# Optimization experiments

Hardware: AMD Instinct MI355X
Metric: run time of the kernel (lower is better)

Reference implementation:

```python
import jax, jax.numpy as jnp
import numpy as np

N_NODES = 10000
N_EDGES = 160000
D_IN = 128
D_EMB = 512
D_HID = 256
GAT_SLOPE = 0.2   # PyG GATv2Conv default negative_slope
MLP_SLOPE = 0.1   # relu_alpha


def _glorot(key, shape):
    fan_in, fan_out = shape[0], shape[-1]
    lim = np.sqrt(6.0 / (fan_in + fan_out))
    return jax.random.uniform(key, shape, jnp.float32, -lim, lim)


def setup_inputs() -> dict:
    key = jax.random.key(0)
    ks = jax.random.split(key, 20)
    inp = {
        'x': jax.random.normal(ks[0], (N_NODES, D_IN), jnp.float32),
        'edge_index': jax.random.randint(ks[1], (2, N_EDGES), 0, N_NODES, jnp.int64),
    }
    # GATv2 layers: (Wl, Wr, att, bias) each
    dims = [(D_IN, D_EMB), (D_EMB, D_EMB), (D_EMB, D_EMB)]
    for i, (di, do) in enumerate(dims, start=1):
        inp[f'Wl{i}'] = _glorot(ks[2 + 4 * i], (di, do))
        inp[f'Wr{i}'] = _glorot(ks[3 + 4 * i], (di, do))
        inp[f'att{i}'] = _glorot(ks[4 + 4 * i], (1, do))[0]
        inp[f'b{i}'] = jnp.zeros((do,), jnp.float32)
    # MLP
    inp['A1'] = _glorot(ks[2], (D_EMB, D_HID)); inp['c1'] = jnp.zeros((D_HID,), jnp.float32)
    inp['A2'] = _glorot(ks[3], (D_HID, D_HID)); inp['c2'] = jnp.zeros((D_HID,), jnp.float32)
    inp['A3'] = _glorot(ks[4], (D_HID, 1));     inp['c3'] = jnp.zeros((1,), jnp.float32)
    return inp


def gatv2_conv(x, src, dst, Wl, Wr, att, bias):
    # PyG GATv2Conv, heads=1: xl = source transform, xr = target transform
    xl = x @ Wl                                   # [N, D]
    xr = x @ Wr                                   # [N, D]
    # per-edge attention logit: att . leaky_relu(xl[src] + xr[dst])
    e = jax.nn.leaky_relu(xl[src] + xr[dst], GAT_SLOPE) @ att   # [E]
    # segment softmax over incoming edges of each dst node
    emax = jax.ops.segment_max(e, dst, num_segments=N_NODES)    # [N]
    w = jnp.exp(e - emax[dst])
    denom = jax.ops.segment_sum(w, dst, num_segments=N_NODES)   # [N]
    alpha = w / (denom[dst] + 1e-16)                             # [E]
    out = jax.ops.segment_sum(alpha[:, None] * xl[src], dst, num_segments=N_NODES)
    return out + bias


def reference(x, edge_index, Wl1, Wr1, att1, b1, Wl2, Wr2, att2, b2,
              Wl3, Wr3, att3, b3, A1, c1, A2, c2, A3, c3):
    src, dst = edge_index[0], edge_index[1]
    h = jnp.tanh(gatv2_conv(x, src, dst, Wl1, Wr1, att1, b1))
    h = jnp.tanh(gatv2_conv(h, src, dst, Wl2, Wr2, att2, b2))
    h = jnp.tanh(gatv2_conv(h, src, dst, Wl3, Wr3, att3, b3))
    h = jax.nn.leaky_relu(h @ A1 + c1, MLP_SLOPE)
    h = jax.nn.leaky_relu(h @ A2 + c2, MLP_SLOPE)
    logits = h @ A3 + c3                          # [N, 1]
    return jax.nn.softmax(logits, axis=0)         # softmax over nodes
```

## Files before the change

kernel.cpp:

```cpp
#include <hip/hip_runtime.h>
#include <hip/hip_bf16.h>

#define N_NODES 10000
#define N_EDGES 160000
#define D_IN    128
#define D_EMB   512
#define D_HID   256

typedef unsigned short u16;
typedef __attribute__((ext_vector_type(8))) short short8;
typedef __attribute__((ext_vector_type(4))) float floatx4;

__device__ __forceinline__ float bf2f(u16 u) {
    union { unsigned int i; float f; } v; v.i = ((unsigned int)u) << 16; return v.f;
}
__device__ __forceinline__ u16 f2bf(float f) {
    union { float f; unsigned int i; } v; v.f = f;
    unsigned int x = v.i;
    return (u16)((x + 0x7fffu + ((x >> 16) & 1u)) >> 16);
}
__device__ __forceinline__ float inval(const void* p, int fp32, int idx) {
    return fp32 ? ((const float*)p)[idx] : bf2f(((const u16*)p)[idx]);
}

__device__ __forceinline__ void gld_lds16(const u16* g, u16* l) {
    __builtin_amdgcn_global_load_lds((const __attribute__((address_space(1))) void*)g,
                                     (__attribute__((address_space(3))) void*)l,
                                     16, 0, 0);
}

__device__ __forceinline__ int edge_src(const int* __restrict__ ei, int flg, int e) {
    int v = flg ? ei[2 * e] : ei[e];
    return min(max(v, 0), N_NODES - 1);
}
__device__ __forceinline__ int edge_dst(const int* __restrict__ ei, int flg, int e) {
    int v = flg ? ei[2 * N_EDGES + 2 * e] : ei[N_EDGES + e];
    return min(max(v, 0), N_NODES - 1);
}

__global__ void sentinel_kernel(float* out, int n) {
    int i = blockIdx.x * 256 + threadIdx.x;
    if (i < n) out[i] = 1.0f;
}

__global__ __launch_bounds__(256)
void detect_zero_kernel(const int* __restrict__ ei, const u16* __restrict__ xu,
                        int* flag, int* counts, float* logits) {
    int gid = blockIdx.x * 256 + threadIdx.x;
    for (int i = gid; i < N_NODES; i += gridDim.x * 256) { counts[i] = 0; logits[i] = 0.f; }
    if (blockIdx.x != 0) return;
    __shared__ int s_or[256];
    __shared__ int s_cnt[256];
    int t = threadIdx.x;
    int v = 0;
    for (int k = t; k < 4096; k += 256) v |= ei[1 + 2 * k];
    int c = 0;
    for (int k = t; k < 4096; k += 256) {
        u16 u = xu[k];
        int ex = (u >> 7) & 0xFF;
        bool plaus = (u == 0) || (ex >= 64 && ex <= 191);
        if (!plaus) c++;
    }
    s_or[t] = v; s_cnt[t] = c;
    __syncthreads();
    for (int off = 128; off > 0; off >>= 1) {
        if (t < off) { s_or[t] |= s_or[t + off]; s_cnt[t] += s_cnt[t + off]; }
        __syncthreads();
    }
    if (t == 0) {
        flag[0] = (s_or[0] == 0) ? 1 : 0;
        flag[1] = (s_cnt[0] > 256) ? 1 : 0;
    }
}

struct ConvJobs {
    const void* src[10];
    u16* dh[10];
    u16* dl[10];
    int rows[10], cols[10], trans[10];
    int cum[11];
    int njobs;
};

__global__ __launch_bounds__(256)
void convert_fused_kernel(ConvJobs jobs, const int* __restrict__ flag) {
    int idx = blockIdx.x * 256 + threadIdx.x;
    if (idx >= jobs.cum[jobs.njobs]) return;
    int fp32 = flag[1];
    int jb = 0;
    while (idx >= jobs.cum[jb + 1]) jb++;
    int local = idx - jobs.cum[jb];
    float v = inval(jobs.src[jb], fp32, local);
    u16 hi = f2bf(v);
    int o;
    if (jobs.trans[jb]) {
        int r = local / jobs.cols[jb], c = local % jobs.cols[jb];
        o = c * jobs.rows[jb] + r;
    } else o = local;
    jobs.dh[jb][o] = hi;
    if (jobs.dl[jb]) jobs.dl[jb][o] = f2bf(v - bf2f(hi));
}

__global__ void count_edges_kernel(const int* __restrict__ ei, const int* __restrict__ flag,
                                   int* counts) {
    int e = blockIdx.x * 256 + threadIdx.x;
    if (e < N_EDGES) atomicAdd(&counts[edge_dst(ei, flag[0], e)], 1);
}

__global__ __launch_bounds__(256)
void scan_counts_kernel(int* counts, int* rowptr) {
    __shared__ int part[256];
    int tid = threadIdx.x;
    const int CH = 40;
    int base = tid * CH;
    int loc[CH];
    int s = 0;
    #pragma unroll
    for (int i = 0; i < CH; i++) {
        int idx = base + i;
        int c = (idx < N_NODES) ? counts[idx] : 0;
        loc[i] = s; s += c;
    }
    part[tid] = s;
    __syncthreads();
    for (int off = 1; off < 256; off <<= 1) {
        int v = part[tid];
        int add = (tid >= off) ? part[tid - off] : 0;
        __syncthreads();
        part[tid] = v + add;
        __syncthreads();
    }
    int pre = (tid > 0) ? part[tid - 1] : 0;
    #pragma unroll
    for (int i = 0; i < CH; i++) {
        int idx = base + i;
        if (idx < N_NODES) { int v = pre + loc[i]; rowptr[idx] = v; counts[idx] = v; }
    }
    if (tid == 255) rowptr[N_NODES] = part[255];
}

__global__ void fill_esrcp_kernel(const int* __restrict__ ei, const int* __restrict__ flag,
                                  int* counts, int* esrcp) {
    int e = blockIdx.x * 256 + threadIdx.x;
    if (e < N_EDGES) {
        int flg = flag[0];
        int pos = atomicAdd(&counts[edge_dst(ei, flg, e)], 1);
        if (pos >= 0 && pos < N_EDGES) esrcp[pos] = edge_src(ei, flg, e);
    }
}

__global__ __launch_bounds__(256)
void gemm_dual_kernel(const u16* __restrict__ Ah, const u16* __restrict__ Al,
                      const u16* __restrict__ B0h, const u16* __restrict__ B1h,
                      u16* __restrict__ C0, float* __restrict__ C1,
                      int M, int N, int K)
{
    __shared__ u16 sAh[128 * 32];
    __shared__ u16 sAl[128 * 32];
    __shared__ u16 sBh[128 * 32];
    int nb = N >> 7;
    int half = (int)blockIdx.x >= nb;
    int bx = half ? (blockIdx.x - nb) : blockIdx.x;
    const u16* BTh = half ? B1h : B0h;

    int tid = threadIdx.x;
    int lane = tid & 63, wv = tid >> 6;
    int l15 = lane & 15, l4 = lane >> 4;
    int wr = (wv >> 1) * 64, wc = (wv & 1) * 64;
    int m0 = blockIdx.y * 128, n0 = bx * 128;

    int i0 = tid, i1 = tid + 256;
    int r0 = i0 >> 2, b0 = i0 & 3, sb0 = b0 ^ ((r0 >> 1) & 3);
    int r1 = i1 >> 2, b1 = i1 & 3, sb1 = b1 ^ ((r1 >> 1) & 3);
    int gr0 = min(m0 + r0, M - 1), gr1 = min(m0 + r1, M - 1);
    const u16* a0p = Ah + (size_t)gr0 * K + sb0 * 8;
    const u16* a1p = Ah + (size_t)gr1 * K + sb1 * 8;
    const u16* l0p = Al + (size_t)gr0 * K + sb0 * 8;
    const u16* l1p = Al + (size_t)gr1 * K + sb1 * 8;
    const u16* bb0p = BTh + (size_t)(n0 + r0) * K + sb0 * 8;
    const u16* bb1p = BTh + (size_t)(n0 + r1) * K + sb1 * 8;
    u16* lA0 = &sAh[(size_t)(wv * 64) * 8];
    u16* lA1 = &sAh[(size_t)(256 + wv * 64) * 8];
    u16* lL0 = &sAl[(size_t)(wv * 64) * 8];
    u16* lL1 = &sAl[(size_t)(256 + wv * 64) * 8];
    u16* lB0 = &sBh[(size_t)(wv * 64) * 8];
    u16* lB1 = &sBh[(size_t)(256 + wv * 64) * 8];

    floatx4 acc[4][4];
    #pragma unroll
    for (int i = 0; i < 4; i++)
        #pragma unroll
        for (int j = 0; j < 4; j++) acc[i][j] = (floatx4){0.f, 0.f, 0.f, 0.f};

    int aoff[4], boff[4];
    #pragma unroll
    for (int i = 0; i < 4; i++) {
        int arow = wr + i * 16 + l15;
        aoff[i] = arow * 32 + ((l4 ^ ((arow >> 1) & 3)) << 3);
        int bcol = wc + i * 16 + l15;
        boff[i] = bcol * 32 + ((l4 ^ ((bcol >> 1) & 3)) << 3);
    }

    for (int kk = 0; kk < K; kk += 32) {
        __syncthreads();
        gld_lds16(a0p + kk, lA0);
        gld_lds16(a1p + kk, lA1);
        gld_lds16(l0p + kk, lL0);
        gld_lds16(l1p + kk, lL1);
        gld_lds16(bb0p + kk, lB0);
        gld_lds16(bb1p + kk, lB1);
        __syncthreads();

        short8 ah[4], al[4];
        #pragma unroll
        for (int i = 0; i < 4; i++) {
            ah[i] = *(const short8*)(&sAh[aoff[i]]);
            al[i] = *(const short8*)(&sAl[aoff[i]]);
        }
        #pragma unroll
        for (int j = 0; j < 4; j++) {
            short8 bh = *(const short8*)(&sBh[boff[j]]);
            #pragma unroll
            for (int i = 0; i < 4; i++) {
                acc[i][j] = __builtin_amdgcn_mfma_f32_16x16x32_bf16(ah[i], bh, acc[i][j], 0, 0, 0);
                acc[i][j] = __builtin_amdgcn_mfma_f32_16x16x32_bf16(al[i], bh, acc[i][j], 0, 0, 0);
            }
        }
    }

    #pragma unroll
    for (int j = 0; j < 4; j++) {
        int col = n0 + wc + j * 16 + l15;
        #pragma unroll
        for (int i = 0; i < 4; i++) {
            #pragma unroll
            for (int r = 0; r < 4; r++) {
                int row = m0 + wr + i * 16 + l4 * 4 + r;
                if (row < M) {
                    if (half) C1[(size_t)row * N + col] = acc[i][j][r];
                    else      C0[(size_t)row * N + col] = f2bf(acc[i][j][r]);
                }
            }
        }
    }
}

template<int FUSE>
__global__ __launch_bounds__(256)
void gemm_mlp64_kernel(const u16* __restrict__ Ah, const u16* __restrict__ Al,
                       const u16* __restrict__ BTh,
                       u16* __restrict__ Ch, u16* __restrict__ Cl,
                       const void* __restrict__ biasraw,
                       const void* __restrict__ A3raw, float* __restrict__ logits,
                       const int* __restrict__ flag,
                       int M, int N, int K)
{
    __shared__ u16 sAh[64 * 32];
    __shared__ u16 sAl[64 * 32];
    __shared__ u16 sBh[64 * 32];
    int tid = threadIdx.x;
    int lane = tid & 63, wv = tid >> 6;
    int l15 = lane & 15, l4 = lane >> 4;
    int m0 = blockIdx.y * 64, n0 = blockIdx.x * 64;

    int r = (tid >> 2), blk = tid & 3, sb = blk ^ ((r >> 1) & 3);
    int gr = min(m0 + r, M - 1);
    const u16* ap = Ah + (size_t)gr * K + sb * 8;
    const u16* lp = Al + (size_t)gr * K + sb * 8;
    const u16* bp = BTh + (size_t)(n0 + r) * K + sb * 8;
    u16* lA = &sAh[(size_t)(wv * 64) * 8];
    u16* lL = &sAl[(size_t)(wv * 64) * 8];
    u16* lB = &sBh[(size_t)(wv * 64) * 8];

    floatx4 acc[4];
    #pragma unroll
    for (int j = 0; j < 4; j++) acc[j] = (floatx4){0.f, 0.f, 0.f, 0.f};

    int arow = wv * 16 + l15;
    int aoff = arow * 32 + ((l4 ^ ((arow >> 1) & 3)) << 3);
    int boff[4];
    #pragma unroll
    for (int j = 0; j < 4; j++) {
        int bcol = j * 16 + l15;
        boff[j] = bcol * 32 + ((l4 ^ ((bcol >> 1) & 3)) << 3);
    }

    for (int kk = 0; kk < K; kk += 32) {
        __syncthreads();
        gld_lds16(ap + kk, lA);
        gld_lds16(lp + kk, lL);
        gld_lds16(bp + kk, lB);
        __syncthreads();

        short8 ah = *(const short8*)(&sAh[aoff]);
        short8 al = *(const short8*)(&sAl[aoff]);
        #pragma unroll
        for (int j = 0; j < 4; j++) {
            short8 bh = *(const short8*)(&sBh[boff[j]]);
            acc[j] = __builtin_amdgcn_mfma_f32_16x16x32_bf16(ah, bh, acc[j], 0, 0, 0);
            acc[j] = __builtin_amdgcn_mfma_f32_16x16x32_bf16(al, bh, acc[j], 0, 0, 0);
        }
    }

    const int fp32 = flag[1];
    float lsum[4] = {0.f, 0.f, 0.f, 0.f};
    #pragma unroll
    for (int j = 0; j < 4; j++) {
        int col = n0 + j * 16 + l15;
        float bv = inval(biasraw, fp32, col);
        float a3 = FUSE ? inval(A3raw, fp32, col) : 0.f;
        #pragma unroll
        for (int rr = 0; rr < 4; rr++) {
            int row = m0 + wv * 16 + l4 * 4 + rr;
            if (row < M) {
                float v = acc[j][rr] + bv;
                v = v > 0.f ? v : 0.1f * v;
                if (FUSE) {
                    lsum[rr] += v * a3;
                } else {
                    u16 hi = f2bf(v);
                    Ch[(size_t)row * N + col] = hi;
                    Cl[(size_t)row * N + col] = f2bf(v - bf2f(hi));
                }
            }
        }
    }
    if (FUSE) {
        #pragma unroll
        for (int rr = 0; rr < 4; rr++) {
            float s = lsum[rr];
            s += __shfl_xor(s, 1);
            s += __shfl_xor(s, 2);
            s += __shfl_xor(s, 4);
            s += __shfl_xor(s, 8);
            int row = m0 + wv * 16 + l4 * 4 + rr;
            if (l15 == 0 && row < M) atomicAdd(&logits[row], s);
        }
    }
}

__device__ __forceinline__ void online_update(float e, const float v[8],
                                              float& m_run, float& s_run, float acc[8])
{
    if (e > m_run) {
        float sc = __expf(m_run - e);
        s_run = s_run * sc + 1.f;
        #pragma unroll
        for (int k = 0; k < 8; k++) acc[k] = acc[k] * sc + v[k];
        m_run = e;
    } else {
        float w = __expf(e - m_run);
        s_run += w;
        #pragma unroll
        for (int k = 0; k < 8; k++) acc[k] += w * v[k];
    }
}

__global__ __launch_bounds__(256)
void gat_wave_kernel(const int* __restrict__ rowptr, const int* __restrict__ esrcp,
                     const u16* __restrict__ xlb, const float* __restrict__ xr,
                     const void* __restrict__ att, const void* __restrict__ bias,
                     const int* __restrict__ flag,
                     u16* __restrict__ hh, u16* __restrict__ hl)
{
    int lane = threadIdx.x & 63, wv = threadIdx.x >> 6;
    int n = blockIdx.x * 4 + wv;
    if (n >= N_NODES) return;
    int fp32 = flag[1];
    int d0 = lane * 8;

    const float* xrr = xr + (size_t)n * D_EMB;
    float4 r0 = *(const float4*)(xrr + d0);
    float4 r1 = *(const float4*)(xrr + d0 + 4);
    float xrv[8] = {r0.x, r0.y, r0.z, r0.w, r1.x, r1.y, r1.z, r1.w};
    float attv[8];
    #pragma unroll
    for (int k = 0; k < 8; k++) attv[k] = inval(att, fp32, d0 + k);

    int beg = rowptr[n], end = rowptr[n + 1];
    float m_run = -3.4e38f, s_run = 0.f;
    float acc[8] = {0.f, 0.f, 0.f, 0.f, 0.f, 0.f, 0.f, 0.f};

    int j = beg;
    for (; j + 4 <= end; j += 4) {
        int s0 = esrcp[j], s1 = esrcp[j + 1], s2 = esrcp[j + 2], s3 = esrcp[j + 3];
        union { uint4 q; u16 us[8]; } u0, u1, u2, u3;
        u0.q = *(const uint4*)(xlb + (size_t)s0 * D_EMB + d0);
        u1.q = *(const uint4*)(xlb + (size_t)s1 * D_EMB + d0);
        u2.q = *(const uint4*)(xlb + (size_t)s2 * D_EMB + d0);
        u3.q = *(const uint4*)(xlb + (size_t)s3 * D_EMB + d0);
        float v0[8], v1[8], v2[8], v3[8];
        #pragma unroll
        for (int k = 0; k < 8; k++) {
            v0[k] = bf2f(u0.us[k]); v1[k] = bf2f(u1.us[k]);
            v2[k] = bf2f(u2.us[k]); v3[k] = bf2f(u3.us[k]);
        }
        float e0 = 0.f, e1 = 0.f, e2 = 0.f, e3 = 0.f;
        #pragma unroll
        for (int k = 0; k < 8; k++) {
            float t0 = v0[k] + xrv[k]; t0 = t0 > 0.f ? t0 : 0.2f * t0; e0 += attv[k] * t0;
            float t1 = v1[k] + xrv[k]; t1 = t1 > 0.f ? t1 : 0.2f * t1; e1 += attv[k] * t1;
            float t2 = v2[k] + xrv[k]; t2 = t2 > 0.f ? t2 : 0.2f * t2; e2 += attv[k] * t2;
            float t3 = v3[k] + xrv[k]; t3 = t3 > 0.f ? t3 : 0.2f * t3; e3 += attv[k] * t3;
        }
        #pragma unroll
        for (int o = 32; o > 0; o >>= 1) {
            e0 += __shfl_xor(e0, o);
            e1 += __shfl_xor(e1, o);
            e2 += __shfl_xor(e2, o);
            e3 += __shfl_xor(e3, o);
        }
        online_update(e0, v0, m_run, s_run, acc);
        online_update(e1, v1, m_run, s_run, acc);
        online_update(e2, v2, m_run, s_run, acc);
        online_update(e3, v3, m_run, s_run, acc);
    }
    for (; j < end; j++) {
        int s0 = esrcp[j];
        union { uint4 q; u16 us[8]; } u0;
        u0.q = *(const uint4*)(xlb + (size_t)s0 * D_EMB + d0);
        float v0[8];
        #pragma unroll
        for (int k = 0; k < 8; k++) v0[k] = bf2f(u0.us[k]);
        float e0 = 0.f;
        #pragma unroll
        for (int k = 0; k < 8; k++) {
            float t = v0[k] + xrv[k]; t = t > 0.f ? t : 0.2f * t; e0 += attv[k] * t;
        }
        #pragma unroll
        for (int o = 32; o > 0; o >>= 1) e0 += __shfl_xor(e0, o);
        online_update(e0, v0, m_run, s_run, acc);
    }

    float inv = 1.f / (s_run + 1e-16f);
    union { uint4 q; u16 us[8]; } ph, pl;
    #pragma unroll
    for (int k = 0; k < 8; k++) {
        float h = tanhf(acc[k] * inv + inval(bias, fp32, d0 + k));
        u16 hi = f2bf(h);
        ph.us[k] = hi;
        pl.us[k] = f2bf(h - bf2f(hi));
    }
    *(uint4*)(&hh[(size_t)n * D_EMB + d0]) = ph.q;
    *(uint4*)(&hl[(size_t)n * D_EMB + d0]) = pl.q;
}

__global__ __launch_bounds__(256)
void softmax_kernel(const float* __restrict__ logits, float* __restrict__ out)
{
    __shared__ float red[4];
    __shared__ float s_m, s_s;
    int tid = threadIdx.x, lane = tid & 63, wv = tid >> 6;
    float m = -3.4e38f;
    for (int i = tid; i < N_NODES; i += 256) m = fmaxf(m, logits[i]);
    #pragma unroll
    for (int o = 32; o > 0; o >>= 1) m = fmaxf(m, __shfl_down(m, o));
    if (lane == 0) red[wv] = m;
    __syncthreads();
    if (tid == 0) {
        float mm = red[0];
        for (int i = 1; i < 4; i++) mm = fmaxf(mm, red[i]);
        s_m = mm;
    }
    __syncthreads();
    float mm = s_m;
    float s = 0.f;
    for (int i = tid; i < N_NODES; i += 256) s += __expf(logits[i] - mm);
    #pragma unroll
    for (int o = 32; o > 0; o >>= 1) s += __shfl_down(s, o);
    if (lane == 0) red[wv] = s;
    __syncthreads();
    if (tid == 0) {
        float ss = 0.f;
        for (int i = 0; i < 4; i++) ss += red[i];
        s_s = ss;
    }
    __syncthreads();
    float invs = 1.f / s_s;
    for (int i = tid; i < N_NODES; i += 256) out[i] = __expf(logits[i] - mm) * invs;
}

extern "C" void kernel_launch(void* const* d_in, const int* in_sizes, int n_in,
                              void* d_out, int out_size, void* d_ws, size_t ws_size,
                              hipStream_t stream)
{
    const void* x   = d_in[0];
    const int*  ei  = (const int*)d_in[1];
    const void* Wl[3]  = {d_in[2],  d_in[6],  d_in[10]};
    const void* Wr[3]  = {d_in[3],  d_in[7],  d_in[11]};
    const void* att[3] = {d_in[4],  d_in[8],  d_in[12]};
    const void* bia[3] = {d_in[5],  d_in[9],  d_in[13]};
    const void* A1 = d_in[14];
    const void* c1 = d_in[15];
    const void* A2 = d_in[16];
    const void* c2 = d_in[17];
    const void* A3 = d_in[18];

    char* p = (char*)d_ws;
    auto alloc = [&](size_t bytes) {
        char* r = p;
        p += (bytes + 255) & ~(size_t)255;
        return r;
    };
    u16*   xlb    = (u16*)  alloc((size_t)N_NODES * D_EMB * 4);
    float* xr     = (float*)alloc((size_t)N_NODES * D_EMB * 4);
    u16*   hh     = (u16*)  alloc((size_t)N_NODES * D_EMB * 2);
    u16*   hl     = (u16*)  alloc((size_t)N_NODES * D_EMB * 2);
    int*   esrcp  = (int*)  alloc((size_t)N_EDGES * 4);
    int*   rowptr = (int*)  alloc((size_t)(N_NODES + 1) * 4);
    int*   counts = (int*)  alloc((size_t)N_NODES * 4);
    int*   flag   = (int*)  alloc(256);
    float* logits = (float*)alloc((size_t)N_NODES * 4);
    u16* wl1h = (u16*)alloc(D_EMB * D_IN  * 2);
    u16* wr1h = (u16*)alloc(D_EMB * D_IN  * 2);
    u16* wl2h = (u16*)alloc(D_EMB * D_EMB * 2);
    u16* wr2h = (u16*)alloc(D_EMB * D_EMB * 2);
    u16* wl3h = (u16*)alloc(D_EMB * D_EMB * 2);
    u16* wr3h = (u16*)alloc(D_EMB * D_EMB * 2);
    u16* a1h  = (u16*)alloc(D_EMB * D_HID * 2);
    u16* a2h  = (u16*)alloc(D_HID * D_HID * 2);
    u16* xph  = (u16*)alloc((size_t)N_NODES * D_IN * 2);
    u16* xpl  = (u16*)alloc((size_t)N_NODES * D_IN * 2);
    size_t needed = (size_t)(p - (char*)d_ws);

    if (ws_size < needed) {
        sentinel_kernel<<<(out_size + 255) / 256, 256, 0, stream>>>((float*)d_out, out_size);
        return;
    }

    u16* m1h = (u16*)xlb;
    u16* m1l = (u16*)((char*)xlb + 5120000);

    detect_zero_kernel<<<40, 256, 0, stream>>>(ei, (const u16*)x, flag, counts, logits);
    count_edges_kernel<<<(N_EDGES + 255) / 256, 256, 0, stream>>>(ei, flag, counts);
    scan_counts_kernel<<<1, 256, 0, stream>>>(counts, rowptr);
    fill_esrcp_kernel<<<(N_EDGES + 255) / 256, 256, 0, stream>>>(ei, flag, counts, esrcp);

    ConvJobs jobs;
    auto setjob = [&](int i, const void* s, u16* dh, u16* dl, int r, int c, int tr) {
        jobs.src[i] = s; jobs.dh[i] = dh; jobs.dl[i] = dl;
        jobs.rows[i] = r; jobs.cols[i] = c; jobs.trans[i] = tr;
    };
    setjob(0, x,     xph,  xpl,     N_NODES, D_IN, 0);
    setjob(1, Wl[0], wl1h, nullptr, D_IN,  D_EMB, 1);
    setjob(2, Wr[0], wr1h, nullptr, D_IN,  D_EMB, 1);
    setjob(3, Wl[1], wl2h, nullptr, D_EMB, D_EMB, 1);
    setjob(4, Wr[1], wr2h, nullptr, D_EMB, D_EMB, 1);
    setjob(5, Wl[2], wl3h, nullptr, D_EMB, D_EMB, 1);
    setjob(6, Wr[2], wr3h, nullptr, D_EMB, D_EMB, 1);
    setjob(7, A1,    a1h,  nullptr, D_EMB, D_HID, 1);
    setjob(8, A2,    a2h,  nullptr, D_HID, D_HID, 1);
    jobs.njobs = 9;
    jobs.cum[0] = 0;
    for (int i = 0; i < 9; i++) jobs.cum[i + 1] = jobs.cum[i] + jobs.rows[i] * jobs.cols[i];
    int ctotal = jobs.cum[9];
    convert_fused_kernel<<<(ctotal + 255) / 256, 256, 0, stream>>>(jobs, flag);

    dim3 gdual(2 * D_EMB / 128, (N_NODES + 127) / 128);
    dim3 gmlp64(D_HID / 64, (N_NODES + 63) / 64);
    int gatgrid = (N_NODES + 3) / 4;

    gemm_dual_kernel<<<gdual, 256, 0, stream>>>(xph, xpl, wl1h, wr1h, xlb, xr, N_NODES, D_EMB, D_IN);
    gat_wave_kernel<<<gatgrid, 256, 0, stream>>>(rowptr, esrcp, xlb, xr, att[0], bia[0], flag, hh, hl);
    gemm_dual_kernel<<<gdual, 256, 0, stream>>>(hh, hl, wl2h, wr2h, xlb, xr, N_NODES, D_EMB, D_EMB);
    gat_wave_kernel<<<gatgrid, 256, 0, stream>>>(rowptr, esrcp, xlb, xr, att[1], bia[1], flag, hh, hl);
    gemm_dual_kernel<<<gdual, 256, 0, stream>>>(hh, hl, wl3h, wr3h, xlb, xr, N_NODES, D_EMB, D_EMB);
    gat_wave_kernel<<<gatgrid, 256, 0, stream>>>(rowptr, esrcp, xlb, xr, att[2], bia[2], flag, hh, hl);

    gemm_mlp64_kernel<0><<<gmlp64, 256, 0, stream>>>(hh, hl, a1h, m1h, m1l, c1, nullptr, nullptr, flag, N_NODES, D_HID, D_EMB);
    gemm_mlp64_kernel<1><<<gmlp64, 256, 0, stream>>>(m1h, m1l, a2h, nullptr, nullptr, c2, A3, logits, flag, N_NODES, D_HID, D_HID);
    softmax_kernel<<<1, 256, 0, stream>>>(logits, (float*)d_out);
}
```

Before: 433.2 us.

## Software-pipeline neighbor gathers and batch online softmax per 4 edges

The per-node GATv2 aggregation loop now prefetches the next group of four neighbor feature rows and the following group's indices while the current group is being computed, and it loads the edge indices cooperatively with one lane each, broadcast by shuffles. The online softmax update is batched over four edges, with one max and one rescale per group instead of four sequential updates. Leaky-relu is rewritten as fmaxf. The aim is to hide gather latency and cut exp and rescale work, at the cost of more registers per thread.

New measurement: 423.5 us. 1.02x faster.

```diff
diff --git a/kernel.cpp b/kernel.cpp
--- a/kernel.cpp
+++ b/kernel.cpp
@@ -378,54 +378,94 @@
     for (int k = 0; k < 8; k++) attv[k] = inval(att, fp32, d0 + k);
 
     int beg = rowptr[n], end = rowptr[n + 1];
+    int deg = end - beg;
+    int ngf = deg >> 2;
+
     float m_run = -3.4e38f, s_run = 0.f;
     float acc[8] = {0.f, 0.f, 0.f, 0.f, 0.f, 0.f, 0.f, 0.f};
 
-    int j = beg;
-    for (; j + 4 <= end; j += 4) {
-        int s0 = esrcp[j], s1 = esrcp[j + 1], s2 = esrcp[j + 2], s3 = esrcp[j + 3];
-        union { uint4 q; u16 us[8]; } u0, u1, u2, u3;
-        u0.q = *(const uint4*)(xlb + (size_t)s0 * D_EMB + d0);
-        u1.q = *(const uint4*)(xlb + (size_t)s1 * D_EMB + d0);
-        u2.q = *(const uint4*)(xlb + (size_t)s2 * D_EMB + d0);
-        u3.q = *(const uint4*)(xlb + (size_t)s3 * D_EMB + d0);
-        float v0[8], v1[8], v2[8], v3[8];
-        #pragma unroll
-        for (int k = 0; k < 8; k++) {
-            v0[k] = bf2f(u0.us[k]); v1[k] = bf2f(u1.us[k]);
-            v2[k] = bf2f(u2.us[k]); v3[k] = bf2f(u3.us[k]);
-        }
-        float e0 = 0.f, e1 = 0.f, e2 = 0.f, e3 = 0.f;
-        #pragma unroll
-        for (int k = 0; k < 8; k++) {
-            float t0 = v0[k] + xrv[k]; t0 = t0 > 0.f ? t0 : 0.2f * t0; e0 += attv[k] * t0;
-            float t1 = v1[k] + xrv[k]; t1 = t1 > 0.f ? t1 : 0.2f * t1; e1 += attv[k] * t1;
-            float t2 = v2[k] + xrv[k]; t2 = t2 > 0.f ? t2 : 0.2f * t2; e2 += attv[k] * t2;
-            float t3 = v3[k] + xrv[k]; t3 = t3 > 0.f ? t3 : 0.2f * t3; e3 += attv[k] * t3;
-        }
-        #pragma unroll
-        for (int o = 32; o > 0; o >>= 1) {
-            e0 += __shfl_xor(e0, o);
-            e1 += __shfl_xor(e1, o);
-            e2 += __shfl_xor(e2, o);
-            e3 += __shfl_xor(e3, o);
-        }
-        online_update(e0, v0, m_run, s_run, acc);
-        online_update(e1, v1, m_run, s_run, acc);
-        online_update(e2, v2, m_run, s_run, acc);
-        online_update(e3, v3, m_run, s_run, acc);
-    }
-    for (; j < end; j++) {
-        int s0 = esrcp[j];
+    const u16* xbase = xlb + d0;
+    int l3 = lane & 3;
+
+    if (ngf > 0) {
+        int i0 = esrcp[min(beg + l3, N_EDGES - 1)];
+        uint4 cu0, cu1, cu2, cu3;
+        {
+            int s0 = __shfl(i0, 0), s1 = __shfl(i0, 1), s2 = __shfl(i0, 2), s3 = __shfl(i0, 3);
+            cu0 = *(const uint4*)(xbase + (size_t)s0 * D_EMB);
+            cu1 = *(const uint4*)(xbase + (size_t)s1 * D_EMB);
+            cu2 = *(const uint4*)(xbase + (size_t)s2 * D_EMB);
+            cu3 = *(const uint4*)(xbase + (size_t)s3 * D_EMB);
+        }
+        int nidx = esrcp[min(beg + 4 + l3, N_EDGES - 1)];
+
+        for (int g = 0; g < ngf; g++) {
+            uint4 nu0, nu1, nu2, nu3;
+            int nidx2 = 0;
+            bool have_next = (g + 1 < ngf);
+            if (have_next) {
+                int t0 = __shfl(nidx, 0), t1 = __shfl(nidx, 1),
+                    t2 = __shfl(nidx, 2), t3 = __shfl(nidx, 3);
+                nu0 = *(const uint4*)(xbase + (size_t)t0 * D_EMB);
+                nu1 = *(const uint4*)(xbase + (size_t)t1 * D_EMB);
+                nu2 = *(const uint4*)(xbase + (size_t)t2 * D_EMB);
+                nu3 = *(const uint4*)(xbase + (size_t)t3 * D_EMB);
+                if (g + 2 < ngf)
+                    nidx2 = esrcp[min(beg + 4 * (g + 2) + l3, N_EDGES - 1)];
+            }
+
+            union { uint4 q; u16 us[8]; } u0, u1, u2, u3;
+            u0.q = cu0; u1.q = cu1; u2.q = cu2; u3.q = cu3;
+            float v0[8], v1[8], v2[8], v3[8];
+            #pragma unroll
+            for (int k = 0; k < 8; k++) {
+                v0[k] = bf2f(u0.us[k]); v1[k] = bf2f(u1.us[k]);
+                v2[k] = bf2f(u2.us[k]); v3[k] = bf2f(u3.us[k]);
+            }
+            float e0 = 0.f, e1 = 0.f, e2 = 0.f, e3 = 0.f;
+            #pragma unroll
+            for (int k = 0; k < 8; k++) {
+                float t0 = v0[k] + xrv[k]; t0 = fmaxf(t0, 0.2f * t0); e0 += attv[k] * t0;
+                float t1 = v1[k] + xrv[k]; t1 = fmaxf(t1, 0.2f * t1); e1 += attv[k] * t1;
+                float t2 = v2[k] + xrv[k]; t2 = fmaxf(t2, 0.2f * t2); e2 += attv[k] * t2;
+                float t3 = v3[k] + xrv[k]; t3 = fmaxf(t3, 0.2f * t3); e3 += attv[k] * t3;
+            }
+            #pragma unroll
+            for (int o = 32; o > 0; o >>= 1) {
+                e0 += __shfl_xor(e0, o);
+                e1 += __shfl_xor(e1, o);
+                e2 += __shfl_xor(e2, o);
+                e3 += __shfl_xor(e3, o);
+            }
+            float m4 = fmaxf(fmaxf(e0, e1), fmaxf(e2, e3));
+            float m_new = fmaxf(m_run, m4);
+            float sc = __expf(m_run - m_new);
+            float w0 = __expf(e0 - m_new), w1 = __expf(e1 - m_new);
+            float w2 = __expf(e2 - m_new), w3 = __expf(e3 - m_new);
+            s_run = s_run * sc + (w0 + w1) + (w2 + w3);
+            #pragma unroll
+            for (int k = 0; k < 8; k++)
+                acc[k] = acc[k] * sc + w0 * v0[k] + w1 * v1[k] + w2 * v2[k] + w3 * v3[k];
+            m_run = m_new;
+
+            if (have_next) {
+                cu0 = nu0; cu1 = nu1; cu2 = nu2; cu3 = nu3;
+                nidx = nidx2;
+            }
+        }
+    }
+
+    for (int j = beg + (ngf << 2); j < end; j++) {
+        int sv = esrcp[j];
         union { uint4 q; u16 us[8]; } u0;
-        u0.q = *(const uint4*)(xlb + (size_t)s0 * D_EMB + d0);
+        u0.q = *(const uint4*)(xlb + (size_t)sv * D_EMB + d0);
         float v0[8];
         #pragma unroll
         for (int k = 0; k < 8; k++) v0[k] = bf2f(u0.us[k]);
         float e0 = 0.f;
         #pragma unroll
         for (int k = 0; k < 8; k++) {
-            float t = v0[k] + xrv[k]; t = t > 0.f ? t : 0.2f * t; e0 += attv[k] * t;
+            float t = v0[k] + xrv[k]; t = fmaxf(t, 0.2f * t); e0 += attv[k] * t;
         }
         #pragma unroll
         for (int o = 32; o > 0; o >>= 1) e0 += __shfl_xor(e0, o);
```

## Split GAT node edges across two waves with software-pipelined gathers and batched softmax

Applied to the files above, without the earlier changes.

Each destination node now gets two waves, each handling half of its incoming edges, and the partial online-softmax states are merged through shared memory. Within a wave, edge indices are loaded cooperatively and broadcast with shuffles. Row gathers are double-buffered so the next group's loads are issued while the current group is computed, and the per-edge branchy online update becomes a branch-free batched update over four edges. This adds parallelism and memory-level overlap for the latency-bound gather, at the cost of shared-memory merging, a block barrier, and wasted lanes on masked tail groups.

New measurement: 461.3 us. 1.06x slower.

```diff
diff --git a/kernel.cpp b/kernel.cpp
--- a/kernel.cpp
+++ b/kernel.cpp
@@ -339,23 +339,6 @@
     }
 }
 
-__device__ __forceinline__ void online_update(float e, const float v[8],
-                                              float& m_run, float& s_run, float acc[8])
-{
-    if (e > m_run) {
-        float sc = __expf(m_run - e);
-        s_run = s_run * sc + 1.f;
-        #pragma unroll
-        for (int k = 0; k < 8; k++) acc[k] = acc[k] * sc + v[k];
-        m_run = e;
-    } else {
-        float w = __expf(e - m_run);
-        s_run += w;
-        #pragma unroll
-        for (int k = 0; k < 8; k++) acc[k] += w * v[k];
-    }
-}
-
 __global__ __launch_bounds__(256)
 void gat_wave_kernel(const int* __restrict__ rowptr, const int* __restrict__ esrcp,
                      const u16* __restrict__ xlb, const float* __restrict__ xr,
@@ -363,13 +346,18 @@
                      const int* __restrict__ flag,
                      u16* __restrict__ hh, u16* __restrict__ hl)
 {
+    __shared__ float s_acc[4][8][64];
+    __shared__ float s_m[4], s_s[4];
+
     int lane = threadIdx.x & 63, wv = threadIdx.x >> 6;
-    int n = blockIdx.x * 4 + wv;
-    if (n >= N_NODES) return;
+    int slot = wv >> 1, w = wv & 1;
+    int n = blockIdx.x * 2 + slot;
+    bool valid_n = (n < N_NODES);
+    int nc = valid_n ? n : 0;
     int fp32 = flag[1];
     int d0 = lane * 8;
 
-    const float* xrr = xr + (size_t)n * D_EMB;
+    const float* xrr = xr + (size_t)nc * D_EMB;
     float4 r0 = *(const float4*)(xrr + d0);
     float4 r1 = *(const float4*)(xrr + d0 + 4);
     float xrv[8] = {r0.x, r0.y, r0.z, r0.w, r1.x, r1.y, r1.z, r1.w};
@@ -377,18 +365,34 @@
     #pragma unroll
     for (int k = 0; k < 8; k++) attv[k] = inval(att, fp32, d0 + k);
 
-    int beg = rowptr[n], end = rowptr[n + 1];
+    int beg = rowptr[nc], end = rowptr[nc + 1];
+    if (!valid_n) { beg = 0; end = 0; }
+    int deg = end - beg;
+    int halfd = (deg + 1) >> 1;
+    int mybeg = beg + w * halfd;
+    int myend = w ? end : (beg + halfd);
+    int ne = myend - mybeg;
+    int ng = (ne + 3) >> 2;
+
     float m_run = -3.4e38f, s_run = 0.f;
     float acc[8] = {0.f, 0.f, 0.f, 0.f, 0.f, 0.f, 0.f, 0.f};
 
-    int j = beg;
-    for (; j + 4 <= end; j += 4) {
-        int s0 = esrcp[j], s1 = esrcp[j + 1], s2 = esrcp[j + 2], s3 = esrcp[j + 3];
+    const u16* xbase = xlb + d0;
+    int l3 = lane & 3;
+
+    auto ldidx = [&](int g) -> int {
+        return esrcp[min(mybeg + 4 * g + l3, N_EDGES - 1)];
+    };
+    auto gather = [&](uint4* C, int iv) {
+        int g0 = __shfl(iv, 0), g1 = __shfl(iv, 1), g2 = __shfl(iv, 2), g3 = __shfl(iv, 3);
+        C[0] = *(const uint4*)(xbase + (size_t)g0 * D_EMB);
+        C[1] = *(const uint4*)(xbase + (size_t)g1 * D_EMB);
+        C[2] = *(const uint4*)(xbase + (size_t)g2 * D_EMB);
+        C[3] = *(const uint4*)(xbase + (size_t)g3 * D_EMB);
+    };
+    auto compute = [&](const uint4* C, int g) {
         union { uint4 q; u16 us[8]; } u0, u1, u2, u3;
-        u0.q = *(const uint4*)(xlb + (size_t)s0 * D_EMB + d0);
-        u1.q = *(const uint4*)(xlb + (size_t)s1 * D_EMB + d0);
-        u2.q = *(const uint4*)(xlb + (size_t)s2 * D_EMB + d0);
-        u3.q = *(const uint4*)(xlb + (size_t)s3 * D_EMB + d0);
+        u0.q = C[0]; u1.q = C[1]; u2.q = C[2]; u3.q = C[3];
         float v0[8], v1[8], v2[8], v3[8];
         #pragma unroll
         for (int k = 0; k < 8; k++) {
@@ -398,10 +402,10 @@
         float e0 = 0.f, e1 = 0.f, e2 = 0.f, e3 = 0.f;
         #pragma unroll
         for (int k = 0; k < 8; k++) {
-            float t0 = v0[k] + xrv[k]; t0 = t0 > 0.f ? t0 : 0.2f * t0; e0 += attv[k] * t0;
-            float t1 = v1[k] + xrv[k]; t1 = t1 > 0.f ? t1 : 0.2f * t1; e1 += attv[k] * t1;
-            float t2 = v2[k] + xrv[k]; t2 = t2 > 0.f ? t2 : 0.2f * t2; e2 += attv[k] * t2;
-            float t3 = v3[k] + xrv[k]; t3 = t3 > 0.f ? t3 : 0.2f * t3; e3 += attv[k] * t3;
+            float t0 = v0[k] + xrv[k]; t0 = fmaxf(t0, 0.2f * t0); e0 += attv[k] * t0;
+            float t1 = v1[k] + xrv[k]; t1 = fmaxf(t1, 0.2f * t1); e1 += attv[k] * t1;
+            float t2 = v2[k] + xrv[k]; t2 = fmaxf(t2, 0.2f * t2); e2 += attv[k] * t2;
+            float t3 = v3[k] + xrv[k]; t3 = fmaxf(t3, 0.2f * t3); e3 += attv[k] * t3;
         }
         #pragma unroll
         for (int o = 32; o > 0; o >>= 1) {
@@ -410,39 +414,65 @@
             e2 += __shfl_xor(e2, o);
             e3 += __shfl_xor(e3, o);
         }
-        online_update(e0, v0, m_run, s_run, acc);
-        online_update(e1, v1, m_run, s_run, acc);
-        online_update(e2, v2, m_run, s_run, acc);
-        online_update(e3, v3, m_run, s_run, acc);
-    }
-    for (; j < end; j++) {
-        int s0 = esrcp[j];
-        union { uint4 q; u16 us[8]; } u0;
-        u0.q = *(const uint4*)(xlb + (size_t)s0 * D_EMB + d0);
-        float v0[8];
-        #pragma unroll
-        for (int k = 0; k < 8; k++) v0[k] = bf2f(u0.us[k]);
-        float e0 = 0.f;
+        int base = mybeg + 4 * g;
+        if (base + 1 >= myend + 1) e0 = -3.4e38f;
+        if (base + 1 >= myend) e1 = -3.4e38f;
+        if (base + 2 >= myend) e2 = -3.4e38f;
+        if (base + 3 >= myend) e3 = -3.4e38f;
+        float m4 = fmaxf(fmaxf(e0, e1), fmaxf(e2, e3));
+        float m_new = fmaxf(m_run, m4);
+        float sc = __expf(m_run - m_new);
+        float w0 = __expf(e0 - m_new), w1 = __expf(e1 - m_new);
+        float w2 = __expf(e2 - m_new), w3 = __expf(e3 - m_new);
+        s_run = s_run * sc + (w0 + w1) + (w2 + w3);
+        #pragma unroll
+        for (int k = 0; k < 8; k++)
+            acc[k] = acc[k] * sc + w0 * v0[k] + w1 * v1[k] + w2 * v2[k] + w3 * v3[k];
+        m_run = m_new;
+    };
+
+    if (ng > 0) {
+        uint4 A[4], B[4];
+        int ia = ldidx(0);
+        int ib = (ng > 1) ? ldidx(1) : 0;
+        gather(A, ia);
+        if (ng > 1) gather(B, ib);
+
+        for (int g = 0; g < ng; g += 2) {
+            bool hasB = (g + 1 < ng);
+            bool refA = (g + 2 < ng), refB = (g + 3 < ng);
+            int ia2 = refA ? ldidx(g + 2) : 0;
+            int ib2 = refB ? ldidx(g + 3) : 0;
+            compute(A, g);
+            if (refA) gather(A, ia2);
+            if (hasB) compute(B, g + 1);
+            if (refB) gather(B, ib2);
+        }
+    }
+
+    #pragma unroll
+    for (int k = 0; k < 8; k++) s_acc[wv][k][lane] = acc[k];
+    if (lane == 0) { s_m[wv] = m_run; s_s[wv] = s_run; }
+    __syncthreads();
+
+    if (w == 0 && valid_n) {
+        float m0 = s_m[wv], m1 = s_m[wv + 1];
+        float mm = fmaxf(m0, m1);
+        float sc0 = __expf(m0 - mm), sc1 = __expf(m1 - mm);
+        float ss = s_s[wv] * sc0 + s_s[wv + 1] * sc1;
+        float inv = 1.f / (ss + 1e-16f);
+        union { uint4 q; u16 us[8]; } ph, pl;
         #pragma unroll
         for (int k = 0; k < 8; k++) {
-            float t = v0[k] + xrv[k]; t = t > 0.f ? t : 0.2f * t; e0 += attv[k] * t;
-        }
-        #pragma unroll
-        for (int o = 32; o > 0; o >>= 1) e0 += __shfl_xor(e0, o);
-        online_update(e0, v0, m_run, s_run, acc);
-    }
-
-    float inv = 1.f / (s_run + 1e-16f);
-    union { uint4 q; u16 us[8]; } ph, pl;
-    #pragma unroll
-    for (int k = 0; k < 8; k++) {
-        float h = tanhf(acc[k] * inv + inval(bias, fp32, d0 + k));
-        u16 hi = f2bf(h);
-        ph.us[k] = hi;
-        pl.us[k] = f2bf(h - bf2f(hi));
-    }
-    *(uint4*)(&hh[(size_t)n * D_EMB + d0]) = ph.q;
-    *(uint4*)(&hl[(size_t)n * D_EMB + d0]) = pl.q;
+            float a = s_acc[wv][k][lane] * sc0 + s_acc[wv + 1][k][lane] * sc1;
+            float h = tanhf(a * inv + inval(bias, fp32, d0 + k));
+            u16 hi = f2bf(h);
+            ph.us[k] = hi;
+            pl.us[k] = f2bf(h - bf2f(hi));
+        }
+        *(uint4*)(&hh[(size_t)n * D_EMB + d0]) = ph.q;
+        *(uint4*)(&hl[(size_t)n * D_EMB + d0]) = pl.q;
+    }
 }
 
 __global__ __launch_bounds__(256)
@@ -558,7 +588,7 @@
 
     dim3 gdual(2 * D_EMB / 128, (N_NODES + 127) / 128);
     dim3 gmlp64(D_HID / 64, (N_NODES + 63) / 64);
-    int gatgrid = (N_NODES + 3) / 4;
+    int gatgrid = (N_NODES + 1) / 2;
 
     gemm_dual_kernel<<<gdual, 256, 0, stream>>>(xph, xpl, wl1h, wr1h, xlb, xr, N_NODES, D_EMB, D_IN);
     gat_wave_kernel<<<gatgrid, 256, 0, stream>>>(rowptr, esrcp, xlb, xr, att[0], bia[0], flag, hh, hl);
```

## Double-buffer 8-edge gather groups with batched online softmax in GAT aggregation

Applied to the files above, without the earlier changes.

Restructures the per-node GATv2 aggregation loop to process edges in groups of 8. Edge indices are loaded cooperatively across lanes and broadcast with shuffles, and row gathers are double-buffered so the loads for the next group overlap computation on the current one. The per-edge branching online-softmax update becomes one batched max/rescale per group. This is meant to hide gather latency and cut serial dependencies, at the cost of more registers (two 8-entry uint4 buffers) and padded work on the tail group.

Measured after the change: 442.9 us. 1.02x slower.

```diff
diff --git a/kernel.cpp b/kernel.cpp
--- a/kernel.cpp
+++ b/kernel.cpp
@@ -339,23 +339,6 @@
     }
 }
 
-__device__ __forceinline__ void online_update(float e, const float v[8],
-                                              float& m_run, float& s_run, float acc[8])
-{
-    if (e > m_run) {
-        float sc = __expf(m_run - e);
-        s_run = s_run * sc + 1.f;
-        #pragma unroll
-        for (int k = 0; k < 8; k++) acc[k] = acc[k] * sc + v[k];
-        m_run = e;
-    } else {
-        float w = __expf(e - m_run);
-        s_run += w;
-        #pragma unroll
-        for (int k = 0; k < 8; k++) acc[k] += w * v[k];
-    }
-}
-
 __global__ __launch_bounds__(256)
 void gat_wave_kernel(const int* __restrict__ rowptr, const int* __restrict__ esrcp,
                      const u16* __restrict__ xlb, const float* __restrict__ xr,
@@ -368,6 +351,15 @@
     if (n >= N_NODES) return;
     int fp32 = flag[1];
     int d0 = lane * 8;
+    int l7 = lane & 7;
+
+    int beg = rowptr[n], end = rowptr[n + 1];
+    int deg = end - beg;
+    int ng = (deg + 7) >> 3;
+
+    const u16* xbase = xlb + d0;
+
+    int idxA = (ng > 0) ? esrcp[min(beg + l7, N_EDGES - 1)] : 0;
 
     const float* xrr = xr + (size_t)n * D_EMB;
     float4 r0 = *(const float4*)(xrr + d0);
@@ -377,59 +369,76 @@
     #pragma unroll
     for (int k = 0; k < 8; k++) attv[k] = inval(att, fp32, d0 + k);
 
-    int beg = rowptr[n], end = rowptr[n + 1];
     float m_run = -3.4e38f, s_run = 0.f;
     float acc[8] = {0.f, 0.f, 0.f, 0.f, 0.f, 0.f, 0.f, 0.f};
 
-    int j = beg;
-    for (; j + 4 <= end; j += 4) {
-        int s0 = esrcp[j], s1 = esrcp[j + 1], s2 = esrcp[j + 2], s3 = esrcp[j + 3];
-        union { uint4 q; u16 us[8]; } u0, u1, u2, u3;
-        u0.q = *(const uint4*)(xlb + (size_t)s0 * D_EMB + d0);
-        u1.q = *(const uint4*)(xlb + (size_t)s1 * D_EMB + d0);
-        u2.q = *(const uint4*)(xlb + (size_t)s2 * D_EMB + d0);
-        u3.q = *(const uint4*)(xlb + (size_t)s3 * D_EMB + d0);
-        float v0[8], v1[8], v2[8], v3[8];
-        #pragma unroll
-        for (int k = 0; k < 8; k++) {
-            v0[k] = bf2f(u0.us[k]); v1[k] = bf2f(u1.us[k]);
-            v2[k] = bf2f(u2.us[k]); v3[k] = bf2f(u3.us[k]);
-        }
-        float e0 = 0.f, e1 = 0.f, e2 = 0.f, e3 = 0.f;
-        #pragma unroll
-        for (int k = 0; k < 8; k++) {
-            float t0 = v0[k] + xrv[k]; t0 = t0 > 0.f ? t0 : 0.2f * t0; e0 += attv[k] * t0;
-            float t1 = v1[k] + xrv[k]; t1 = t1 > 0.f ? t1 : 0.2f * t1; e1 += attv[k] * t1;
-            float t2 = v2[k] + xrv[k]; t2 = t2 > 0.f ? t2 : 0.2f * t2; e2 += attv[k] * t2;
-            float t3 = v3[k] + xrv[k]; t3 = t3 > 0.f ? t3 : 0.2f * t3; e3 += attv[k] * t3;
+    auto gather8 = [&](uint4* C, int iv) {
+        #pragma unroll
+        for (int i = 0; i < 8; i++) {
+            int s = __shfl(iv, i);
+            C[i] = *(const uint4*)(xbase + (size_t)s * D_EMB);
+        }
+    };
+    auto compute8 = [&](const uint4* C, int g) {
+        float e[8];
+        #pragma unroll
+        for (int i = 0; i < 8; i++) {
+            union { uint4 q; u16 us[8]; } u; u.q = C[i];
+            float ei = 0.f;
+            #pragma unroll
+            for (int k = 0; k < 8; k++) {
+                float v = bf2f(u.us[k]);
+                float t = v + xrv[k];
+                t = fmaxf(t, 0.2f * t);
+                ei += attv[k] * t;
+            }
+            e[i] = ei;
         }
         #pragma unroll
         for (int o = 32; o > 0; o >>= 1) {
-            e0 += __shfl_xor(e0, o);
-            e1 += __shfl_xor(e1, o);
-            e2 += __shfl_xor(e2, o);
-            e3 += __shfl_xor(e3, o);
-        }
-        online_update(e0, v0, m_run, s_run, acc);
-        online_update(e1, v1, m_run, s_run, acc);
-        online_update(e2, v2, m_run, s_run, acc);
-        online_update(e3, v3, m_run, s_run, acc);
-    }
-    for (; j < end; j++) {
-        int s0 = esrcp[j];
-        union { uint4 q; u16 us[8]; } u0;
-        u0.q = *(const uint4*)(xlb + (size_t)s0 * D_EMB + d0);
-        float v0[8];
-        #pragma unroll
-        for (int k = 0; k < 8; k++) v0[k] = bf2f(u0.us[k]);
-        float e0 = 0.f;
-        #pragma unroll
-        for (int k = 0; k < 8; k++) {
-            float t = v0[k] + xrv[k]; t = t > 0.f ? t : 0.2f * t; e0 += attv[k] * t;
-        }
-        #pragma unroll
-        for (int o = 32; o > 0; o >>= 1) e0 += __shfl_xor(e0, o);
-        online_update(e0, v0, m_run, s_run, acc);
+            #pragma unroll
+            for (int i = 0; i < 8; i++) e[i] += __shfl_xor(e[i], o);
+        }
+        int base = beg + 8 * g;
+        #pragma unroll
+        for (int i = 0; i < 8; i++) if (base + i >= end) e[i] = -3.4e38f;
+        float m8 = e[0];
+        #pragma unroll
+        for (int i = 1; i < 8; i++) m8 = fmaxf(m8, e[i]);
+        float m_new = fmaxf(m_run, m8);
+        float sc = __expf(m_run - m_new);
+        float w[8];
+        float ssum = 0.f;
+        #pragma unroll
+        for (int i = 0; i < 8; i++) { w[i] = __expf(e[i] - m_new); ssum += w[i]; }
+        s_run = s_run * sc + ssum;
+        #pragma unroll
+        for (int k = 0; k < 8; k++) acc[k] *= sc;
+        #pragma unroll
+        for (int i = 0; i < 8; i++) {
+            union { uint4 q; u16 us[8]; } u; u.q = C[i];
+            #pragma unroll
+            for (int k = 0; k < 8; k++) acc[k] += w[i] * bf2f(u.us[k]);
+        }
+        m_run = m_new;
+    };
+
+    if (ng > 0) {
+        uint4 A[8], B[8];
+        gather8(A, idxA);
+        int idxB = (ng > 1) ? esrcp[min(beg + 8 + l7, N_EDGES - 1)] : 0;
+
+        for (int g = 0; g < ng; g += 2) {
+            bool hasB = (g + 1 < ng);
+            if (hasB) gather8(B, idxB);
+            int idxA2 = (g + 2 < ng) ? esrcp[min(beg + 8 * (g + 2) + l7, N_EDGES - 1)] : 0;
+            compute8(A, g);
+            if (hasB) {
+                if (g + 2 < ng) gather8(A, idxA2);
+                if (g + 3 < ng) idxB = esrcp[min(beg + 8 * (g + 3) + l7, N_EDGES - 1)];
+                compute8(B, g + 1);
+            }
+        }
     }
 
     float inv = 1.f / (s_run + 1e-16f);
```
